# Performance work log

Measured on AMD Instinct MI355X. Metric: run time of the kernel, lower is better.

## Reference

```python
import jax, jax.numpy as jnp
import numpy as np

NUM_EXPERTS = 32
HIDDEN = 2048
INTER = 768
TOP_K = 4
B, S = 2, 512


def setup_inputs() -> dict:
    key = jax.random.key(0)
    k1, k2, k3, k4, k5 = jax.random.split(key, 5)
    hidden_states = jax.random.normal(k1, (B, S, HIDDEN), dtype=jnp.float32)
    routing_weights = jax.random.uniform(k2, (B, S, NUM_EXPERTS), dtype=jnp.float32)
    gate_up_proj = jax.random.normal(k3, (NUM_EXPERTS, HIDDEN, 2 * INTER), dtype=jnp.float32) * 0.02
    down_proj = jax.random.normal(k4, (NUM_EXPERTS, INTER, HIDDEN), dtype=jnp.float32) * 0.02
    router_indices = jax.random.randint(k5, (B, S, TOP_K), 0, NUM_EXPERTS, dtype=jnp.int64)
    return {
        "hidden_states": hidden_states,
        "routing_weights": routing_weights,
        "gate_up_proj": gate_up_proj,
        "down_proj": down_proj,
        "router_indices": router_indices,
    }


def reference(hidden_states, routing_weights, gate_up_proj, down_proj, router_indices):
    b, s, h = hidden_states.shape
    e = gate_up_proj.shape[0]
    x = hidden_states.reshape(-1, h)                       # [T, H]
    ri = router_indices.reshape(-1, router_indices.shape[-1])  # [T, K]
    rw = routing_weights.reshape(-1, e)                    # [T, E]
    # token-expert membership: expert applied once per token iff it appears in top-k
    member = (ri[:, :, None] == jnp.arange(e)[None, None, :]).any(axis=1)  # [T, E] bool
    combine_w = jnp.where(member, rw, 0.0)                 # [T, E]
    # dense grouped-GEMM reference: compute every expert for every token, mask-combine
    gate_up = jnp.einsum("th,ehg->teg", x, gate_up_proj)   # [T, E, 2I]
    gate, up = jnp.split(gate_up, 2, axis=-1)              # [T, E, I] each
    act = jax.nn.silu(gate) * up                           # SwiGLU
    act = act * combine_w[:, :, None]                      # fold combine weights pre-down-proj
    out = jnp.einsum("tei,eih->th", act, down_proj)        # [T, H]
    return out.reshape(b, s, h)
```

## Files before the change

### kernel.cpp

```cpp
#include <hip/hip_runtime.h>
#include <hip/hip_bf16.h>

#define NUM_EXPERTS 32
#define HIDDEN 2048
#define INTER 768
#define TOPK 4
#define T_TOKENS 1024
#define CAP 1024

#define MT 64
#define BK 64
#define LSTR 72

typedef __bf16 bf16x8 __attribute__((ext_vector_type(8)));
typedef float floatx4 __attribute__((ext_vector_type(4)));

__device__ __forceinline__ int swz(int row, int kq) {
    return row * LSTR + (((kq ^ (row >> 2)) & 7) << 3);
}

__global__ void route_kernel(const int* __restrict__ ri, int* __restrict__ counts,
                             int* __restrict__ tok_list) {
    int t = blockIdx.x * blockDim.x + threadIdx.x;
    if (t >= T_TOKENS) return;
    int idx[TOPK];
#pragma unroll
    for (int j = 0; j < TOPK; ++j) idx[j] = ri[t * TOPK + j];
#pragma unroll
    for (int j = 0; j < TOPK; ++j) {
        int e = idx[j];
        bool dup = false;
#pragma unroll
        for (int l = 0; l < TOPK; ++l)
            if (l < j && idx[l] == e) dup = true;
        if (!dup) {
            int s = atomicAdd(&counts[e], 1);
            tok_list[e * CAP + s] = t;
        }
    }
}

__global__ __launch_bounds__(256) void gemm1_kernel(
    const float* __restrict__ x, const float* __restrict__ rw,
    const float* __restrict__ Wgu, const int* __restrict__ counts,
    const int* __restrict__ tok_list, __bf16* __restrict__ act) {
    const int e = blockIdx.y;
    const int zi = blockIdx.x % 3;
    const int n0 = (blockIdx.x / 3) * 64;
    const int count = counts[e];
    const int tid = threadIdx.x;
    const int wave = tid >> 6;
    const int lane = tid & 63;
    const int fr = lane & 15;
    const int fq = lane >> 4;
    const int wr = wave >> 1;
    const int wc = wave & 1;

    __shared__ int s_off;
    __shared__ int s_tok[MT];
    __shared__ float s_w[MT];
    __shared__ __align__(16) __bf16 As[MT * LSTR];
    __shared__ __align__(16) __bf16 Bs[128 * LSTR];

    if (tid == 0) {
        int o = 0;
        for (int i = 0; i < e; ++i) o += counts[i];
        s_off = o;
    }

    const size_t wbase = (size_t)e * HIDDEN * (2 * INTER);

    const int ng = (tid & 31) * 4;
    const int kg = tid >> 5;
    const int bwc = ng >> 6;
    const int bj = ng & 63;
    const int memcol = (bj < 32) ? (n0 + bwc * 32 + bj)
                                 : (INTER + n0 + bwc * 32 + (bj - 32));
    const int ar = tid >> 2;
    const int aq = tid & 3;

    for (int m0 = zi * MT; m0 < count; m0 += 3 * MT) {
        __syncthreads();
        if (tid < MT) {
            int slot = m0 + tid;
            int t = (slot < count) ? tok_list[e * CAP + slot] : tok_list[e * CAP];
            s_tok[tid] = t;
            s_w[tid] = (slot < count) ? rw[t * NUM_EXPERTS + e] : 0.f;
        }
        __syncthreads();

        const float* aRow = x + (size_t)s_tok[ar] * HIDDEN + aq * 16;
        const float* bCol = Wgu + wbase + (size_t)(kg * 8) * (2 * INTER) + memcol;

        float4 pa[4], pb[8];
        auto loadA = [&](int kbase) {
            const float4* s = (const float4*)(aRow + kbase);
#pragma unroll
            for (int i = 0; i < 4; ++i) pa[i] = s[i];
        };
        auto loadB = [&](int kbase) {
#pragma unroll
            for (int r8 = 0; r8 < 8; ++r8)
                pb[r8] = *(const float4*)(bCol + (size_t)(kbase + r8) * (2 * INTER));
        };
        auto writeA = [&]() {
            bf16x8 p0, p1;
            p0[0] = (__bf16)pa[0].x; p0[1] = (__bf16)pa[0].y; p0[2] = (__bf16)pa[0].z; p0[3] = (__bf16)pa[0].w;
            p0[4] = (__bf16)pa[1].x; p0[5] = (__bf16)pa[1].y; p0[6] = (__bf16)pa[1].z; p0[7] = (__bf16)pa[1].w;
            p1[0] = (__bf16)pa[2].x; p1[1] = (__bf16)pa[2].y; p1[2] = (__bf16)pa[2].z; p1[3] = (__bf16)pa[2].w;
            p1[4] = (__bf16)pa[3].x; p1[5] = (__bf16)pa[3].y; p1[6] = (__bf16)pa[3].z; p1[7] = (__bf16)pa[3].w;
            *(bf16x8*)&As[swz(ar, 2 * aq)] = p0;
            *(bf16x8*)&As[swz(ar, 2 * aq + 1)] = p1;
        };
        auto writeB = [&]() {
#pragma unroll
            for (int c = 0; c < 4; ++c) {
                bf16x8 p;
#pragma unroll
                for (int r8 = 0; r8 < 8; ++r8)
                    p[r8] = (__bf16)((const float*)&pb[r8])[c];
                *(bf16x8*)&Bs[swz(ng + c, kg)] = p;
            }
        };

        floatx4 acc[2][4];
#pragma unroll
        for (int ms = 0; ms < 2; ++ms)
#pragma unroll
            for (int nf = 0; nf < 4; ++nf)
                acc[ms][nf] = (floatx4){0.f, 0.f, 0.f, 0.f};

        loadA(0); loadB(0);
        writeA(); writeB();
        __syncthreads();

        for (int k0 = 0; k0 < HIDDEN; k0 += BK) {
            const bool has_next = (k0 + BK < HIDDEN);
            if (has_next) { loadA(k0 + BK); loadB(k0 + BK); }

#pragma unroll
            for (int ks = 0; ks < 2; ++ks) {
                bf16x8 af[2], bf[4];
#pragma unroll
                for (int ms = 0; ms < 2; ++ms)
                    af[ms] = *(const bf16x8*)&As[swz(wr * 32 + ms * 16 + fr, ks * 4 + fq)];
#pragma unroll
                for (int nf = 0; nf < 4; ++nf)
                    bf[nf] = *(const bf16x8*)&Bs[swz(wc * 64 + nf * 16 + fr, ks * 4 + fq)];
#pragma unroll
                for (int ms = 0; ms < 2; ++ms)
#pragma unroll
                    for (int nf = 0; nf < 4; ++nf)
                        acc[ms][nf] = __builtin_amdgcn_mfma_f32_16x16x32_bf16(af[ms], bf[nf], acc[ms][nf], 0, 0, 0);
            }
            __syncthreads();
            if (has_next) { writeA(); writeB(); }
            __syncthreads();
        }

        const int off = s_off;
#pragma unroll
        for (int ms = 0; ms < 2; ++ms) {
            int rbase = wr * 32 + ms * 16 + fq * 4;
#pragma unroll
            for (int i = 0; i < 4; ++i) {
                int slot = m0 + rbase + i;
                if (slot < count) {
                    float w = s_w[rbase + i];
#pragma unroll
                    for (int nf = 0; nf < 2; ++nf) {
                        float gv = acc[ms][nf][i];
                        float uv = acc[ms][nf + 2][i];
                        float a = gv / (1.f + __expf(-gv)) * uv * w;
                        act[(size_t)(off + slot) * INTER + n0 + wc * 32 + nf * 16 + fr] = (__bf16)a;
                    }
                }
            }
        }
    }
}

__global__ __launch_bounds__(256) void gemm2_kernel(
    const __bf16* __restrict__ act, const float* __restrict__ Wd,
    const int* __restrict__ counts, const int* __restrict__ tok_list,
    float* __restrict__ out) {
    const int e = blockIdx.y;
    const int zi = blockIdx.x % 3;
    const int n0 = (blockIdx.x / 3) * 128;
    const int count = counts[e];
    const int tid = threadIdx.x;
    const int wave = tid >> 6;
    const int lane = tid & 63;
    const int fr = lane & 15;
    const int fq = lane >> 4;
    const int wr = wave >> 1;
    const int wc = wave & 1;

    __shared__ int s_off;
    __shared__ int s_tok[MT];
    __shared__ __align__(16) __bf16 As[MT * LSTR];
    __shared__ __align__(16) __bf16 Bs[128 * LSTR];

    if (tid == 0) {
        int o = 0;
        for (int i = 0; i < e; ++i) o += counts[i];
        s_off = o;
    }

    const size_t wbase = (size_t)e * INTER * HIDDEN;
    const int ng = (tid & 31) * 4;
    const int kg = tid >> 5;
    const int ar = tid >> 2;
    const int aq = tid & 3;

    for (int m0 = zi * MT; m0 < count; m0 += 3 * MT) {
        __syncthreads();
        if (tid < MT) {
            int slot = m0 + tid;
            s_tok[tid] = (slot < count) ? tok_list[e * CAP + slot] : 0;
        }
        __syncthreads();

        const __bf16* aRow = act + (size_t)(s_off + min(m0 + ar, count - 1)) * INTER + aq * 16;
        const float* bCol = Wd + wbase + (size_t)(kg * 8) * HIDDEN + n0 + ng;

        bf16x8 qa[2];
        float4 pb[8];
        auto loadA = [&](int kbase) {
            const bf16x8* s = (const bf16x8*)(aRow + kbase);
            qa[0] = s[0];
            qa[1] = s[1];
        };
        auto loadB = [&](int kbase) {
#pragma unroll
            for (int r8 = 0; r8 < 8; ++r8)
                pb[r8] = *(const float4*)(bCol + (size_t)(kbase + r8) * HIDDEN);
        };
        auto writeA = [&]() {
            *(bf16x8*)&As[swz(ar, 2 * aq)] = qa[0];
            *(bf16x8*)&As[swz(ar, 2 * aq + 1)] = qa[1];
        };
        auto writeB = [&]() {
#pragma unroll
            for (int c = 0; c < 4; ++c) {
                bf16x8 p;
#pragma unroll
                for (int r8 = 0; r8 < 8; ++r8)
                    p[r8] = (__bf16)((const float*)&pb[r8])[c];
                *(bf16x8*)&Bs[swz(ng + c, kg)] = p;
            }
        };

        floatx4 acc[2][4];
#pragma unroll
        for (int ms = 0; ms < 2; ++ms)
#pragma unroll
            for (int nf = 0; nf < 4; ++nf)
                acc[ms][nf] = (floatx4){0.f, 0.f, 0.f, 0.f};

        loadA(0); loadB(0);
        writeA(); writeB();
        __syncthreads();

        for (int k0 = 0; k0 < INTER; k0 += BK) {
            const bool has_next = (k0 + BK < INTER);
            if (has_next) { loadA(k0 + BK); loadB(k0 + BK); }

#pragma unroll
            for (int ks = 0; ks < 2; ++ks) {
                bf16x8 af[2], bf[4];
#pragma unroll
                for (int ms = 0; ms < 2; ++ms)
                    af[ms] = *(const bf16x8*)&As[swz(wr * 32 + ms * 16 + fr, ks * 4 + fq)];
#pragma unroll
                for (int nf = 0; nf < 4; ++nf)
                    bf[nf] = *(const bf16x8*)&Bs[swz(wc * 64 + nf * 16 + fr, ks * 4 + fq)];
#pragma unroll
                for (int ms = 0; ms < 2; ++ms)
#pragma unroll
                    for (int nf = 0; nf < 4; ++nf)
                        acc[ms][nf] = __builtin_amdgcn_mfma_f32_16x16x32_bf16(af[ms], bf[nf], acc[ms][nf], 0, 0, 0);
            }
            __syncthreads();
            if (has_next) { writeA(); writeB(); }
            __syncthreads();
        }

#pragma unroll
        for (int ms = 0; ms < 2; ++ms) {
            int rbase = wr * 32 + ms * 16 + fq * 4;
#pragma unroll
            for (int i = 0; i < 4; ++i) {
                int slot = m0 + rbase + i;
                if (slot < count) {
                    int t = s_tok[rbase + i];
#pragma unroll
                    for (int nf = 0; nf < 4; ++nf)
                        atomicAdd(&out[(size_t)t * HIDDEN + n0 + wc * 64 + nf * 16 + fr], acc[ms][nf][i]);
                }
            }
        }
    }
}

extern "C" void kernel_launch(void* const* d_in, const int* in_sizes, int n_in,
                              void* d_out, int out_size, void* d_ws, size_t ws_size,
                              hipStream_t stream) {
    const float* x   = (const float*)d_in[0];
    const float* rw  = (const float*)d_in[1];
    const float* Wgu = (const float*)d_in[2];
    const float* Wd  = (const float*)d_in[3];
    const int*   ri  = (const int*)d_in[4];
    float* out = (float*)d_out;

    int* counts   = (int*)d_ws;
    int* tok_list = (int*)((char*)d_ws + 512);
    __bf16* act   = (__bf16*)((char*)d_ws + 512 + NUM_EXPERTS * CAP * 4);

    hipMemsetAsync(d_ws, 0, 512, stream);
    hipMemsetAsync(d_out, 0, (size_t)T_TOKENS * HIDDEN * sizeof(float), stream);

    route_kernel<<<dim3(T_TOKENS / 256), 256, 0, stream>>>(ri, counts, tok_list);
    gemm1_kernel<<<dim3(3 * INTER / 64, NUM_EXPERTS), 256, 0, stream>>>(x, rw, Wgu, counts, tok_list, act);
    gemm2_kernel<<<dim3(3 * HIDDEN / 128, NUM_EXPERTS), 256, 0, stream>>>(act, Wd, counts, tok_list, out);
}
```

Before: 749.7 us.

## Double-buffer LDS tiles with two-deep register prefetch in both MoE GEMMs

Both grouped GEMM kernels now keep two LDS buffers for the A and B tiles and two register staging sets, so global loads run two k-tiles ahead. The next tile is written to the idle buffer while the MFMA step reads the other one, which leaves one barrier per k-step instead of two. Launch bounds now ask for two blocks per CU. The cost is double the LDS footprint and extra staging registers, which can raise register pressure or cause spills under the two-block bound.

```diff
diff --git a/kernel.cpp b/kernel.cpp
--- a/kernel.cpp
+++ b/kernel.cpp
@@ -11,6 +11,8 @@
 #define MT 64
 #define BK 64
 #define LSTR 72
+#define NT1 (HIDDEN / BK)
+#define NT2 (INTER / BK)
 
 typedef __bf16 bf16x8 __attribute__((ext_vector_type(8)));
 typedef float floatx4 __attribute__((ext_vector_type(4)));
@@ -40,7 +42,7 @@
     }
 }
 
-__global__ __launch_bounds__(256) void gemm1_kernel(
+__global__ __launch_bounds__(256, 2) void gemm1_kernel(
     const float* __restrict__ x, const float* __restrict__ rw,
     const float* __restrict__ Wgu, const int* __restrict__ counts,
     const int* __restrict__ tok_list, __bf16* __restrict__ act) {
@@ -59,8 +61,8 @@
     __shared__ int s_off;
     __shared__ int s_tok[MT];
     __shared__ float s_w[MT];
-    __shared__ __align__(16) __bf16 As[MT * LSTR];
-    __shared__ __align__(16) __bf16 Bs[128 * LSTR];
+    __shared__ __align__(16) __bf16 As[2][MT * LSTR];
+    __shared__ __align__(16) __bf16 Bs[2][128 * LSTR];
 
     if (tid == 0) {
         int o = 0;
@@ -92,34 +94,35 @@
         const float* aRow = x + (size_t)s_tok[ar] * HIDDEN + aq * 16;
         const float* bCol = Wgu + wbase + (size_t)(kg * 8) * (2 * INTER) + memcol;
 
-        float4 pa[4], pb[8];
-        auto loadA = [&](int kbase) {
-            const float4* s = (const float4*)(aRow + kbase);
+        float4 a0[4], a1[4], b0[8], b1[8];
+
+        auto loadA = [&](float4* pa, int kb) {
+            const float4* s = (const float4*)(aRow + kb);
 #pragma unroll
             for (int i = 0; i < 4; ++i) pa[i] = s[i];
         };
-        auto loadB = [&](int kbase) {
+        auto loadB = [&](float4* pb, int kb) {
 #pragma unroll
             for (int r8 = 0; r8 < 8; ++r8)
-                pb[r8] = *(const float4*)(bCol + (size_t)(kbase + r8) * (2 * INTER));
-        };
-        auto writeA = [&]() {
+                pb[r8] = *(const float4*)(bCol + (size_t)(kb + r8) * (2 * INTER));
+        };
+        auto writeA = [&](__bf16* Ad, const float4* pa) {
             bf16x8 p0, p1;
             p0[0] = (__bf16)pa[0].x; p0[1] = (__bf16)pa[0].y; p0[2] = (__bf16)pa[0].z; p0[3] = (__bf16)pa[0].w;
             p0[4] = (__bf16)pa[1].x; p0[5] = (__bf16)pa[1].y; p0[6] = (__bf16)pa[1].z; p0[7] = (__bf16)pa[1].w;
             p1[0] = (__bf16)pa[2].x; p1[1] = (__bf16)pa[2].y; p1[2] = (__bf16)pa[2].z; p1[3] = (__bf16)pa[2].w;
             p1[4] = (__bf16)pa[3].x; p1[5] = (__bf16)pa[3].y; p1[6] = (__bf16)pa[3].z; p1[7] = (__bf16)pa[3].w;
-            *(bf16x8*)&As[swz(ar, 2 * aq)] = p0;
-            *(bf16x8*)&As[swz(ar, 2 * aq + 1)] = p1;
-        };
-        auto writeB = [&]() {
+            *(bf16x8*)&Ad[swz(ar, 2 * aq)] = p0;
+            *(bf16x8*)&Ad[swz(ar, 2 * aq + 1)] = p1;
+        };
+        auto writeB = [&](__bf16* Bd, const float4* pb) {
 #pragma unroll
             for (int c = 0; c < 4; ++c) {
                 bf16x8 p;
 #pragma unroll
                 for (int r8 = 0; r8 < 8; ++r8)
                     p[r8] = (__bf16)((const float*)&pb[r8])[c];
-                *(bf16x8*)&Bs[swz(ng + c, kg)] = p;
+                *(bf16x8*)&Bd[swz(ng + c, kg)] = p;
             }
         };
 
@@ -130,32 +133,44 @@
             for (int nf = 0; nf < 4; ++nf)
                 acc[ms][nf] = (floatx4){0.f, 0.f, 0.f, 0.f};
 
-        loadA(0); loadB(0);
-        writeA(); writeB();
-        __syncthreads();
-
-        for (int k0 = 0; k0 < HIDDEN; k0 += BK) {
-            const bool has_next = (k0 + BK < HIDDEN);
-            if (has_next) { loadA(k0 + BK); loadB(k0 + BK); }
-
+        auto compute = [&](const __bf16* Ad, const __bf16* Bd) {
 #pragma unroll
             for (int ks = 0; ks < 2; ++ks) {
-                bf16x8 af[2], bf[4];
+                bf16x8 af[2], bfr[4];
 #pragma unroll
                 for (int ms = 0; ms < 2; ++ms)
-                    af[ms] = *(const bf16x8*)&As[swz(wr * 32 + ms * 16 + fr, ks * 4 + fq)];
+                    af[ms] = *(const bf16x8*)&Ad[swz(wr * 32 + ms * 16 + fr, ks * 4 + fq)];
 #pragma unroll
                 for (int nf = 0; nf < 4; ++nf)
-                    bf[nf] = *(const bf16x8*)&Bs[swz(wc * 64 + nf * 16 + fr, ks * 4 + fq)];
+                    bfr[nf] = *(const bf16x8*)&Bd[swz(wc * 64 + nf * 16 + fr, ks * 4 + fq)];
 #pragma unroll
                 for (int ms = 0; ms < 2; ++ms)
 #pragma unroll
                     for (int nf = 0; nf < 4; ++nf)
-                        acc[ms][nf] = __builtin_amdgcn_mfma_f32_16x16x32_bf16(af[ms], bf[nf], acc[ms][nf], 0, 0, 0);
-            }
+                        acc[ms][nf] = __builtin_amdgcn_mfma_f32_16x16x32_bf16(af[ms], bfr[nf], acc[ms][nf], 0, 0, 0);
+            }
+        };
+
+        loadA(a0, 0);          loadB(b0, 0);
+        loadA(a1, BK);         loadB(b1, BK);
+        writeA(As[0], a0);     writeB(Bs[0], b0);
+        loadA(a0, 2 * BK);     loadB(b0, 2 * BK);
+        __syncthreads();
+
+        for (int it = 0; it < NT1; it += 2) {
+            if (it + 1 < NT1) {
+                writeA(As[1], a1); writeB(Bs[1], b1);
+                if (it + 3 < NT1) { loadA(a1, (it + 3) * BK); loadB(b1, (it + 3) * BK); }
+            }
+            compute(As[0], Bs[0]);
+            if (it + 1 >= NT1) break;
             __syncthreads();
-            if (has_next) { writeA(); writeB(); }
-            __syncthreads();
+            if (it + 2 < NT1) {
+                writeA(As[0], a0); writeB(Bs[0], b0);
+                if (it + 4 < NT1) { loadA(a0, (it + 4) * BK); loadB(b0, (it + 4) * BK); }
+            }
+            compute(As[1], Bs[1]);
+            if (it + 2 < NT1) __syncthreads();
         }
 
         const int off = s_off;
@@ -180,7 +195,7 @@
     }
 }
 
-__global__ __launch_bounds__(256) void gemm2_kernel(
+__global__ __launch_bounds__(256, 2) void gemm2_kernel(
     const __bf16* __restrict__ act, const float* __restrict__ Wd,
     const int* __restrict__ counts, const int* __restrict__ tok_list,
     float* __restrict__ out) {
@@ -198,8 +213,8 @@
 
     __shared__ int s_off;
     __shared__ int s_tok[MT];
-    __shared__ __align__(16) __bf16 As[MT * LSTR];
-    __shared__ __align__(16) __bf16 Bs[128 * LSTR];
+    __shared__ __align__(16) __bf16 As[2][MT * LSTR];
+    __shared__ __align__(16) __bf16 Bs[2][128 * LSTR];
 
     if (tid == 0) {
         int o = 0;
@@ -224,30 +239,31 @@
         const __bf16* aRow = act + (size_t)(s_off + min(m0 + ar, count - 1)) * INTER + aq * 16;
         const float* bCol = Wd + wbase + (size_t)(kg * 8) * HIDDEN + n0 + ng;
 
-        bf16x8 qa[2];
-        float4 pb[8];
-        auto loadA = [&](int kbase) {
-            const bf16x8* s = (const bf16x8*)(aRow + kbase);
+        bf16x8 qa0[2], qa1[2];
+        float4 b0[8], b1[8];
+
+        auto loadA = [&](bf16x8* qa, int kb) {
+            const bf16x8* s = (const bf16x8*)(aRow + kb);
             qa[0] = s[0];
             qa[1] = s[1];
         };
-        auto loadB = [&](int kbase) {
+        auto loadB = [&](float4* pb, int kb) {
 #pragma unroll
             for (int r8 = 0; r8 < 8; ++r8)
-                pb[r8] = *(const float4*)(bCol + (size_t)(kbase + r8) * HIDDEN);
-        };
-        auto writeA = [&]() {
-            *(bf16x8*)&As[swz(ar, 2 * aq)] = qa[0];
-            *(bf16x8*)&As[swz(ar, 2 * aq + 1)] = qa[1];
-        };
-        auto writeB = [&]() {
+                pb[r8] = *(const float4*)(bCol + (size_t)(kb + r8) * HIDDEN);
+        };
+        auto writeA = [&](__bf16* Ad, const bf16x8* qa) {
+            *(bf16x8*)&Ad[swz(ar, 2 * aq)] = qa[0];
+            *(bf16x8*)&Ad[swz(ar, 2 * aq + 1)] = qa[1];
+        };
+        auto writeB = [&](__bf16* Bd, const float4* pb) {
 #pragma unroll
             for (int c = 0; c < 4; ++c) {
                 bf16x8 p;
 #pragma unroll
                 for (int r8 = 0; r8 < 8; ++r8)
                     p[r8] = (__bf16)((const float*)&pb[r8])[c];
-                *(bf16x8*)&Bs[swz(ng + c, kg)] = p;
+                *(bf16x8*)&Bd[swz(ng + c, kg)] = p;
             }
         };
 
@@ -258,32 +274,44 @@
             for (int nf = 0; nf < 4; ++nf)
                 acc[ms][nf] = (floatx4){0.f, 0.f, 0.f, 0.f};
 
-        loadA(0); loadB(0);
-        writeA(); writeB();
-        __syncthreads();
-
-        for (int k0 = 0; k0 < INTER; k0 += BK) {
-            const bool has_next = (k0 + BK < INTER);
-            if (has_next) { loadA(k0 + BK); loadB(k0 + BK); }
-
+        auto compute = [&](const __bf16* Ad, const __bf16* Bd) {
 #pragma unroll
             for (int ks = 0; ks < 2; ++ks) {
-                bf16x8 af[2], bf[4];
+                bf16x8 af[2], bfr[4];
 #pragma unroll
                 for (int ms = 0; ms < 2; ++ms)
-                    af[ms] = *(const bf16x8*)&As[swz(wr * 32 + ms * 16 + fr, ks * 4 + fq)];
+                    af[ms] = *(const bf16x8*)&Ad[swz(wr * 32 + ms * 16 + fr, ks * 4 + fq)];
 #pragma unroll
                 for (int nf = 0; nf < 4; ++nf)
-                    bf[nf] = *(const bf16x8*)&Bs[swz(wc * 64 + nf * 16 + fr, ks * 4 + fq)];
+                    bfr[nf] = *(const bf16x8*)&Bd[swz(wc * 64 + nf * 16 + fr, ks * 4 + fq)];
 #pragma unroll
                 for (int ms = 0; ms < 2; ++ms)
 #pragma unroll
                     for (int nf = 0; nf < 4; ++nf)
-                        acc[ms][nf] = __builtin_amdgcn_mfma_f32_16x16x32_bf16(af[ms], bf[nf], acc[ms][nf], 0, 0, 0);
-            }
+                        acc[ms][nf] = __builtin_amdgcn_mfma_f32_16x16x32_bf16(af[ms], bfr[nf], acc[ms][nf], 0, 0, 0);
+            }
+        };
+
+        loadA(qa0, 0);          loadB(b0, 0);
+        loadA(qa1, BK);         loadB(b1, BK);
+        writeA(As[0], qa0);     writeB(Bs[0], b0);
+        loadA(qa0, 2 * BK);     loadB(b0, 2 * BK);
+        __syncthreads();
+
+        for (int it = 0; it < NT2; it += 2) {
+            if (it + 1 < NT2) {
+                writeA(As[1], qa1); writeB(Bs[1], b1);
+                if (it + 3 < NT2) { loadA(qa1, (it + 3) * BK); loadB(b1, (it + 3) * BK); }
+            }
+            compute(As[0], Bs[0]);
+            if (it + 1 >= NT2) break;
             __syncthreads();
-            if (has_next) { writeA(); writeB(); }
-            __syncthreads();
+            if (it + 2 < NT2) {
+                writeA(As[0], qa0); writeB(Bs[0], b0);
+                if (it + 4 < NT2) { loadA(qa0, (it + 4) * BK); loadB(b0, (it + 4) * BK); }
+            }
+            compute(As[1], Bs[1]);
+            if (it + 2 < NT2) __syncthreads();
         }
 
 #pragma unroll
```

After: 754.9 us. No clear change (+0.7%).

## Reuse each expert weight tile across up to three token tiles per block

Applied to the files above, without the earlier changes.

Each block now handles up to 192 tokens (three 64-row tiles) against one weight tile, so the fp32 expert weights are loaded and converted to bf16 once instead of once per token tile split across three blocks. The grid shrinks by a factor of three. A separate kernel converts the hidden states to bf16 up front, which halves A-operand traffic in the first GEMM. The cost is more accumulator registers (launch bounds set to 2 blocks per SM), more shared memory, and fewer blocks, which lowers parallelism.

```diff
diff --git a/kernel.cpp b/kernel.cpp
--- a/kernel.cpp
+++ b/kernel.cpp
@@ -8,7 +8,7 @@
 #define T_TOKENS 1024
 #define CAP 1024
 
-#define MT 64
+#define MW 192
 #define BK 64
 #define LSTR 72
 
@@ -40,13 +40,23 @@
     }
 }
 
-__global__ __launch_bounds__(256) void gemm1_kernel(
-    const float* __restrict__ x, const float* __restrict__ rw,
+__global__ __launch_bounds__(256) void conv_kernel(const float* __restrict__ x,
+                                                   __bf16* __restrict__ xb) {
+    int i = (blockIdx.x * 256 + threadIdx.x) * 8;
+    float4 f0 = *(const float4*)(x + i);
+    float4 f1 = *(const float4*)(x + i + 4);
+    bf16x8 p;
+    p[0] = (__bf16)f0.x; p[1] = (__bf16)f0.y; p[2] = (__bf16)f0.z; p[3] = (__bf16)f0.w;
+    p[4] = (__bf16)f1.x; p[5] = (__bf16)f1.y; p[6] = (__bf16)f1.z; p[7] = (__bf16)f1.w;
+    *(bf16x8*)(xb + i) = p;
+}
+
+__global__ __launch_bounds__(256, 2) void gemm1_kernel(
+    const __bf16* __restrict__ xb, const float* __restrict__ rw,
     const float* __restrict__ Wgu, const int* __restrict__ counts,
     const int* __restrict__ tok_list, __bf16* __restrict__ act) {
     const int e = blockIdx.y;
-    const int zi = blockIdx.x % 3;
-    const int n0 = (blockIdx.x / 3) * 64;
+    const int n0 = blockIdx.x * 64;
     const int count = counts[e];
     const int tid = threadIdx.x;
     const int wave = tid >> 6;
@@ -57,9 +67,9 @@
     const int wc = wave & 1;
 
     __shared__ int s_off;
-    __shared__ int s_tok[MT];
-    __shared__ float s_w[MT];
-    __shared__ __align__(16) __bf16 As[MT * LSTR];
+    __shared__ int s_tok[MW];
+    __shared__ float s_w[MW];
+    __shared__ __align__(16) __bf16 As[MW * LSTR];
     __shared__ __align__(16) __bf16 Bs[128 * LSTR];
 
     if (tid == 0) {
@@ -76,41 +86,50 @@
     const int bj = ng & 63;
     const int memcol = (bj < 32) ? (n0 + bwc * 32 + bj)
                                  : (INTER + n0 + bwc * 32 + (bj - 32));
+    const float* bCol = Wgu + wbase + (size_t)(kg * 8) * (2 * INTER) + memcol;
     const int ar = tid >> 2;
     const int aq = tid & 3;
 
-    for (int m0 = zi * MT; m0 < count; m0 += 3 * MT) {
-        __syncthreads();
-        if (tid < MT) {
+    for (int m0 = 0; m0 < count; m0 += MW) {
+        __syncthreads();
+        if (tid < MW) {
             int slot = m0 + tid;
             int t = (slot < count) ? tok_list[e * CAP + slot] : tok_list[e * CAP];
             s_tok[tid] = t;
             s_w[tid] = (slot < count) ? rw[t * NUM_EXPERTS + e] : 0.f;
         }
         __syncthreads();
-
-        const float* aRow = x + (size_t)s_tok[ar] * HIDDEN + aq * 16;
-        const float* bCol = Wgu + wbase + (size_t)(kg * 8) * (2 * INTER) + memcol;
-
-        float4 pa[4], pb[8];
-        auto loadA = [&](int kbase) {
-            const float4* s = (const float4*)(aRow + kbase);
-#pragma unroll
-            for (int i = 0; i < 4; ++i) pa[i] = s[i];
-        };
-        auto loadB = [&](int kbase) {
+        const int nt = min(3, (count - m0 + 63) >> 6);
+
+        const __bf16* aRow[3];
+#pragma unroll
+        for (int mt = 0; mt < 3; ++mt)
+            aRow[mt] = (mt < nt) ? (xb + (size_t)s_tok[mt * 64 + ar] * HIDDEN + aq * 16)
+                                 : xb;
+
+        bf16x8 qa[3][2];
+        float4 qb[8];
+        auto loadA = [&](int kb) {
+#pragma unroll
+            for (int mt = 0; mt < 3; ++mt)
+                if (mt < nt) {
+                    const bf16x8* s = (const bf16x8*)(aRow[mt] + kb);
+                    qa[mt][0] = s[0];
+                    qa[mt][1] = s[1];
+                }
+        };
+        auto loadB = [&](int kb) {
 #pragma unroll
             for (int r8 = 0; r8 < 8; ++r8)
-                pb[r8] = *(const float4*)(bCol + (size_t)(kbase + r8) * (2 * INTER));
+                qb[r8] = *(const float4*)(bCol + (size_t)(kb + r8) * (2 * INTER));
         };
         auto writeA = [&]() {
-            bf16x8 p0, p1;
-            p0[0] = (__bf16)pa[0].x; p0[1] = (__bf16)pa[0].y; p0[2] = (__bf16)pa[0].z; p0[3] = (__bf16)pa[0].w;
-            p0[4] = (__bf16)pa[1].x; p0[5] = (__bf16)pa[1].y; p0[6] = (__bf16)pa[1].z; p0[7] = (__bf16)pa[1].w;
-            p1[0] = (__bf16)pa[2].x; p1[1] = (__bf16)pa[2].y; p1[2] = (__bf16)pa[2].z; p1[3] = (__bf16)pa[2].w;
-            p1[4] = (__bf16)pa[3].x; p1[5] = (__bf16)pa[3].y; p1[6] = (__bf16)pa[3].z; p1[7] = (__bf16)pa[3].w;
-            *(bf16x8*)&As[swz(ar, 2 * aq)] = p0;
-            *(bf16x8*)&As[swz(ar, 2 * aq + 1)] = p1;
+#pragma unroll
+            for (int mt = 0; mt < 3; ++mt)
+                if (mt < nt) {
+                    *(bf16x8*)&As[swz(mt * 64 + ar, 2 * aq)] = qa[mt][0];
+                    *(bf16x8*)&As[swz(mt * 64 + ar, 2 * aq + 1)] = qa[mt][1];
+                }
         };
         auto writeB = [&]() {
 #pragma unroll
@@ -118,75 +137,87 @@
                 bf16x8 p;
 #pragma unroll
                 for (int r8 = 0; r8 < 8; ++r8)
-                    p[r8] = (__bf16)((const float*)&pb[r8])[c];
+                    p[r8] = (__bf16)((const float*)&qb[r8])[c];
                 *(bf16x8*)&Bs[swz(ng + c, kg)] = p;
             }
         };
 
-        floatx4 acc[2][4];
-#pragma unroll
-        for (int ms = 0; ms < 2; ++ms)
-#pragma unroll
-            for (int nf = 0; nf < 4; ++nf)
-                acc[ms][nf] = (floatx4){0.f, 0.f, 0.f, 0.f};
+        floatx4 acc[3][2][4];
+#pragma unroll
+        for (int mt = 0; mt < 3; ++mt)
+#pragma unroll
+            for (int ms = 0; ms < 2; ++ms)
+#pragma unroll
+                for (int nf = 0; nf < 4; ++nf)
+                    acc[mt][ms][nf] = (floatx4){0.f, 0.f, 0.f, 0.f};
 
         loadA(0); loadB(0);
         writeA(); writeB();
         __syncthreads();
 
         for (int k0 = 0; k0 < HIDDEN; k0 += BK) {
-            const bool has_next = (k0 + BK < HIDDEN);
-            if (has_next) { loadA(k0 + BK); loadB(k0 + BK); }
+            const bool hn = (k0 + BK < HIDDEN);
+            if (hn) { loadA(k0 + BK); loadB(k0 + BK); }
 
 #pragma unroll
             for (int ks = 0; ks < 2; ++ks) {
-                bf16x8 af[2], bf[4];
-#pragma unroll
-                for (int ms = 0; ms < 2; ++ms)
-                    af[ms] = *(const bf16x8*)&As[swz(wr * 32 + ms * 16 + fr, ks * 4 + fq)];
+                bf16x8 bfr[4];
 #pragma unroll
                 for (int nf = 0; nf < 4; ++nf)
-                    bf[nf] = *(const bf16x8*)&Bs[swz(wc * 64 + nf * 16 + fr, ks * 4 + fq)];
-#pragma unroll
-                for (int ms = 0; ms < 2; ++ms)
-#pragma unroll
-                    for (int nf = 0; nf < 4; ++nf)
-                        acc[ms][nf] = __builtin_amdgcn_mfma_f32_16x16x32_bf16(af[ms], bf[nf], acc[ms][nf], 0, 0, 0);
+                    bfr[nf] = *(const bf16x8*)&Bs[swz(wc * 64 + nf * 16 + fr, ks * 4 + fq)];
+#pragma unroll
+                for (int mt = 0; mt < 3; ++mt)
+                    if (mt < nt) {
+                        bf16x8 af[2];
+#pragma unroll
+                        for (int ms = 0; ms < 2; ++ms)
+                            af[ms] = *(const bf16x8*)&As[swz(mt * 64 + wr * 32 + ms * 16 + fr, ks * 4 + fq)];
+#pragma unroll
+                        for (int ms = 0; ms < 2; ++ms)
+#pragma unroll
+                            for (int nf = 0; nf < 4; ++nf)
+                                acc[mt][ms][nf] = __builtin_amdgcn_mfma_f32_16x16x32_bf16(
+                                    af[ms], bfr[nf], acc[mt][ms][nf], 0, 0, 0);
+                    }
             }
             __syncthreads();
-            if (has_next) { writeA(); writeB(); }
+            if (hn) { writeA(); writeB(); }
             __syncthreads();
         }
 
         const int off = s_off;
 #pragma unroll
-        for (int ms = 0; ms < 2; ++ms) {
-            int rbase = wr * 32 + ms * 16 + fq * 4;
-#pragma unroll
-            for (int i = 0; i < 4; ++i) {
-                int slot = m0 + rbase + i;
-                if (slot < count) {
-                    float w = s_w[rbase + i];
-#pragma unroll
-                    for (int nf = 0; nf < 2; ++nf) {
-                        float gv = acc[ms][nf][i];
-                        float uv = acc[ms][nf + 2][i];
-                        float a = gv / (1.f + __expf(-gv)) * uv * w;
-                        act[(size_t)(off + slot) * INTER + n0 + wc * 32 + nf * 16 + fr] = (__bf16)a;
+        for (int mt = 0; mt < 3; ++mt)
+            if (mt < nt) {
+                int rbase = mt * 64 + wr * 32;
+#pragma unroll
+                for (int ms = 0; ms < 2; ++ms) {
+                    int rb = rbase + ms * 16 + fq * 4;
+#pragma unroll
+                    for (int i = 0; i < 4; ++i) {
+                        int slot = m0 + rb + i;
+                        if (slot < count) {
+                            float w = s_w[rb + i];
+#pragma unroll
+                            for (int nf = 0; nf < 2; ++nf) {
+                                float gv = acc[mt][ms][nf][i];
+                                float uv = acc[mt][ms][nf + 2][i];
+                                float a = gv / (1.f + __expf(-gv)) * uv * w;
+                                act[(size_t)(off + slot) * INTER + n0 + wc * 32 + nf * 16 + fr] = (__bf16)a;
+                            }
+                        }
                     }
                 }
             }
-        }
-    }
-}
-
-__global__ __launch_bounds__(256) void gemm2_kernel(
+    }
+}
+
+__global__ __launch_bounds__(256, 2) void gemm2_kernel(
     const __bf16* __restrict__ act, const float* __restrict__ Wd,
     const int* __restrict__ counts, const int* __restrict__ tok_list,
     float* __restrict__ out) {
     const int e = blockIdx.y;
-    const int zi = blockIdx.x % 3;
-    const int n0 = (blockIdx.x / 3) * 128;
+    const int n0 = blockIdx.x * 128;
     const int count = counts[e];
     const int tid = threadIdx.x;
     const int wave = tid >> 6;
@@ -197,8 +228,8 @@
     const int wc = wave & 1;
 
     __shared__ int s_off;
-    __shared__ int s_tok[MT];
-    __shared__ __align__(16) __bf16 As[MT * LSTR];
+    __shared__ int s_tok[MW];
+    __shared__ __align__(16) __bf16 As[MW * LSTR];
     __shared__ __align__(16) __bf16 Bs[128 * LSTR];
 
     if (tid == 0) {
@@ -210,35 +241,47 @@
     const size_t wbase = (size_t)e * INTER * HIDDEN;
     const int ng = (tid & 31) * 4;
     const int kg = tid >> 5;
+    const float* bCol = Wd + wbase + (size_t)(kg * 8) * HIDDEN + n0 + ng;
     const int ar = tid >> 2;
     const int aq = tid & 3;
 
-    for (int m0 = zi * MT; m0 < count; m0 += 3 * MT) {
-        __syncthreads();
-        if (tid < MT) {
+    for (int m0 = 0; m0 < count; m0 += MW) {
+        __syncthreads();
+        if (tid < MW) {
             int slot = m0 + tid;
             s_tok[tid] = (slot < count) ? tok_list[e * CAP + slot] : 0;
         }
         __syncthreads();
-
-        const __bf16* aRow = act + (size_t)(s_off + min(m0 + ar, count - 1)) * INTER + aq * 16;
-        const float* bCol = Wd + wbase + (size_t)(kg * 8) * HIDDEN + n0 + ng;
-
-        bf16x8 qa[2];
-        float4 pb[8];
-        auto loadA = [&](int kbase) {
-            const bf16x8* s = (const bf16x8*)(aRow + kbase);
-            qa[0] = s[0];
-            qa[1] = s[1];
-        };
-        auto loadB = [&](int kbase) {
+        const int nt = min(3, (count - m0 + 63) >> 6);
+
+        const __bf16* aRow[3];
+#pragma unroll
+        for (int mt = 0; mt < 3; ++mt)
+            aRow[mt] = act + (size_t)(s_off + min(m0 + mt * 64 + ar, count - 1)) * INTER + aq * 16;
+
+        bf16x8 qa[3][2];
+        float4 qb[8];
+        auto loadA = [&](int kb) {
+#pragma unroll
+            for (int mt = 0; mt < 3; ++mt)
+                if (mt < nt) {
+                    const bf16x8* s = (const bf16x8*)(aRow[mt] + kb);
+                    qa[mt][0] = s[0];
+                    qa[mt][1] = s[1];
+                }
+        };
+        auto loadB = [&](int kb) {
 #pragma unroll
             for (int r8 = 0; r8 < 8; ++r8)
-                pb[r8] = *(const float4*)(bCol + (size_t)(kbase + r8) * HIDDEN);
+                qb[r8] = *(const float4*)(bCol + (size_t)(kb + r8) * HIDDEN);
         };
         auto writeA = [&]() {
-            *(bf16x8*)&As[swz(ar, 2 * aq)] = qa[0];
-            *(bf16x8*)&As[swz(ar, 2 * aq + 1)] = qa[1];
+#pragma unroll
+            for (int mt = 0; mt < 3; ++mt)
+                if (mt < nt) {
+                    *(bf16x8*)&As[swz(mt * 64 + ar, 2 * aq)] = qa[mt][0];
+                    *(bf16x8*)&As[swz(mt * 64 + ar, 2 * aq + 1)] = qa[mt][1];
+                }
         };
         auto writeB = [&]() {
 #pragma unroll
@@ -246,60 +289,73 @@
                 bf16x8 p;
 #pragma unroll
                 for (int r8 = 0; r8 < 8; ++r8)
-                    p[r8] = (__bf16)((const float*)&pb[r8])[c];
+                    p[r8] = (__bf16)((const float*)&qb[r8])[c];
                 *(bf16x8*)&Bs[swz(ng + c, kg)] = p;
             }
         };
 
-        floatx4 acc[2][4];
-#pragma unroll
-        for (int ms = 0; ms < 2; ++ms)
-#pragma unroll
-            for (int nf = 0; nf < 4; ++nf)
-                acc[ms][nf] = (floatx4){0.f, 0.f, 0.f, 0.f};
+        floatx4 acc[3][2][4];
+#pragma unroll
+        for (int mt = 0; mt < 3; ++mt)
+#pragma unroll
+            for (int ms = 0; ms < 2; ++ms)
+#pragma unroll
+                for (int nf = 0; nf < 4; ++nf)
+                    acc[mt][ms][nf] = (floatx4){0.f, 0.f, 0.f, 0.f};
 
         loadA(0); loadB(0);
         writeA(); writeB();
         __syncthreads();
 
         for (int k0 = 0; k0 < INTER; k0 += BK) {
-            const bool has_next = (k0 + BK < INTER);
-            if (has_next) { loadA(k0 + BK); loadB(k0 + BK); }
+            const bool hn = (k0 + BK < INTER);
+            if (hn) { loadA(k0 + BK); loadB(k0 + BK); }
 
 #pragma unroll
             for (int ks = 0; ks < 2; ++ks) {
-                bf16x8 af[2], bf[4];
-#pragma unroll
-                for (int ms = 0; ms < 2; ++ms)
-                    af[ms] = *(const bf16x8*)&As[swz(wr * 32 + ms * 16 + fr, ks * 4 + fq)];
+                bf16x8 bfr[4];
 #pragma unroll
                 for (int nf = 0; nf < 4; ++nf)
-                    bf[nf] = *(const bf16x8*)&Bs[swz(wc * 64 + nf * 16 + fr, ks * 4 + fq)];
-#pragma unroll
-                for (int ms = 0; ms < 2; ++ms)
-#pragma unroll
-                    for (int nf = 0; nf < 4; ++nf)
-                        acc[ms][nf] = __builtin_amdgcn_mfma_f32_16x16x32_bf16(af[ms], bf[nf], acc[ms][nf], 0, 0, 0);
+                    bfr[nf] = *(const bf16x8*)&Bs[swz(wc * 64 + nf * 16 + fr, ks * 4 + fq)];
+#pragma unroll
+                for (int mt = 0; mt < 3; ++mt)
+                    if (mt < nt) {
+                        bf16x8 af[2];
+#pragma unroll
+                        for (int ms = 0; ms < 2; ++ms)
+                            af[ms] = *(const bf16x8*)&As[swz(mt * 64 + wr * 32 + ms * 16 + fr, ks * 4 + fq)];
+#pragma unroll
+                        for (int ms = 0; ms < 2; ++ms)
+#pragma unroll
+                            for (int nf = 0; nf < 4; ++nf)
+                                acc[mt][ms][nf] = __builtin_amdgcn_mfma_f32_16x16x32_bf16(
+                                    af[ms], bfr[nf], acc[mt][ms][nf], 0, 0, 0);
+                    }
             }
             __syncthreads();
-            if (has_next) { writeA(); writeB(); }
+            if (hn) { writeA(); writeB(); }
             __syncthreads();
         }
 
 #pragma unroll
-        for (int ms = 0; ms < 2; ++ms) {
-            int rbase = wr * 32 + ms * 16 + fq * 4;
-#pragma unroll
-            for (int i = 0; i < 4; ++i) {
-                int slot = m0 + rbase + i;
-                if (slot < count) {
-                    int t = s_tok[rbase + i];
-#pragma unroll
-                    for (int nf = 0; nf < 4; ++nf)
-                        atomicAdd(&out[(size_t)t * HIDDEN + n0 + wc * 64 + nf * 16 + fr], acc[ms][nf][i]);
-                }
-            }
-        }
+        for (int mt = 0; mt < 3; ++mt)
+            if (mt < nt) {
+#pragma unroll
+                for (int ms = 0; ms < 2; ++ms) {
+                    int rb = mt * 64 + wr * 32 + ms * 16 + fq * 4;
+#pragma unroll
+                    for (int i = 0; i < 4; ++i) {
+                        int slot = m0 + rb + i;
+                        if (slot < count) {
+                            int t = s_tok[rb + i];
+#pragma unroll
+                            for (int nf = 0; nf < 4; ++nf)
+                                atomicAdd(&out[(size_t)t * HIDDEN + n0 + wc * 64 + nf * 16 + fr],
+                                          acc[mt][ms][nf][i]);
+                        }
+                    }
+                }
+            }
     }
 }
 
@@ -316,11 +372,14 @@
     int* counts   = (int*)d_ws;
     int* tok_list = (int*)((char*)d_ws + 512);
     __bf16* act   = (__bf16*)((char*)d_ws + 512 + NUM_EXPERTS * CAP * 4);
+    __bf16* xb    = (__bf16*)((char*)d_ws + 512 + NUM_EXPERTS * CAP * 4
+                              + (size_t)NUM_EXPERTS * CAP * INTER * 2);
 
     hipMemsetAsync(d_ws, 0, 512, stream);
     hipMemsetAsync(d_out, 0, (size_t)T_TOKENS * HIDDEN * sizeof(float), stream);
 
+    conv_kernel<<<dim3(T_TOKENS * HIDDEN / (256 * 8)), 256, 0, stream>>>(x, xb);
     route_kernel<<<dim3(T_TOKENS / 256), 256, 0, stream>>>(ri, counts, tok_list);
-    gemm1_kernel<<<dim3(3 * INTER / 64, NUM_EXPERTS), 256, 0, stream>>>(x, rw, Wgu, counts, tok_list, act);
-    gemm2_kernel<<<dim3(3 * HIDDEN / 128, NUM_EXPERTS), 256, 0, stream>>>(act, Wd, counts, tok_list, out);
-}
+    gemm1_kernel<<<dim3(INTER / 64, NUM_EXPERTS), 256, 0, stream>>>(xb, rw, Wgu, counts, tok_list, act);
+    gemm2_kernel<<<dim3(HIDDEN / 128, NUM_EXPERTS), 256, 0, stream>>>(act, Wd, counts, tok_list, out);
+}
```

Result: faster. 705.5 us (-5.9%).
